# Kernel optimization log

Measured on AMD Instinct MI355X. Metric: run time of the kernel, lower is better.

## Reference

```python
import jax, jax.numpy as jnp
from jax import lax
import numpy as np

B, T, C, HID, H, W = 8, 24, 3, 32, 64, 64


def setup_inputs() -> dict:
    key = jax.random.key(0)
    ks = jax.random.split(key, 8)
    def n(k, shape, s=0.05):
        return jax.random.normal(k, shape, dtype=jnp.float32) * s
    return {
        "x": n(ks[0], (B, T, C, H, W), 1.0),
        # encoder layer 0: conv over concat(x, h) -> 4*HID gate channels
        "Wenc0": n(ks[1], (4 * HID, C + HID, 3, 3)),
        "benc0": jnp.zeros((4 * HID,), jnp.float32),
        # encoder layer 1: input is layer-0 hidden seq (HID channels)
        "Wenc1": n(ks[2], (4 * HID, HID + HID, 3, 3)),
        "benc1": jnp.zeros((4 * HID,), jnp.float32),
        # decoder (1 layer, input_dim channels in)
        "Wdec": n(ks[3], (4 * HID, C + HID, 3, 3)),
        "bdec": jnp.zeros((4 * HID,), jnp.float32),
        # MLP head: HID*H*W -> 256 -> 97
        "fc1_w": n(ks[4], (256, HID * H * W), 0.01),
        "fc1_b": jnp.zeros((256,), jnp.float32),
        "fc2_w": n(ks[5], (97, 256)),
        "fc2_b": jnp.zeros((97,), jnp.float32),
    }


def _cell_step(h, c, x_t, Wk, b):
    # ConvLSTM cell: conv(concat(x,h)) -> i,f,o,g gates
    z = lax.conv_general_dilated(
        jnp.concatenate([x_t, h], axis=1), Wk,
        window_strides=(1, 1), padding='SAME',
        dimension_numbers=('NCHW', 'OIHW', 'NCHW')) + b[None, :, None, None]
    i, f, o, g = jnp.split(z, 4, axis=1)
    c_new = jax.nn.sigmoid(f) * c + jax.nn.sigmoid(i) * jnp.tanh(g)
    h_new = jax.nn.sigmoid(o) * jnp.tanh(c_new)
    return h_new, c_new


def _run_layer(x_tb, Wk, b):
    # x_tb: [T, B, Cin, H, W]; zero-initialized state
    h0 = jnp.zeros((x_tb.shape[1], HID, H, W), x_tb.dtype)
    c0 = jnp.zeros_like(h0)
    def step(hc, xt):
        h, c = _cell_step(hc[0], hc[1], xt, Wk, b)
        return (h, c), h
    (hT, cT), hs = lax.scan(step, (h0, c0), x_tb)
    return hs, (hT, cT)


def reference(x, Wenc0, benc0, Wenc1, benc1, Wdec, bdec, fc1_w, fc1_b, fc2_w, fc2_b):
    x_tb = jnp.transpose(x, (1, 0, 2, 3, 4))          # [T,B,C,H,W]
    hs0, _ = _run_layer(x_tb, Wenc0, benc0)           # layer-0 hidden seq
    _, (hT, cT) = _run_layer(hs0, Wenc1, benc1)       # last-layer final state
    # decoder: one step on last input frame, seeded with encoder state
    h_dec, _ = _cell_step(hT, cT, x[:, -1], Wdec, bdec)  # [B,HID,H,W]
    feat = h_dec.reshape(h_dec.shape[0], -1)          # [B, HID*H*W]
    hdn = jax.nn.relu(feat @ fc1_w.T + fc1_b)
    return hdn @ fc2_w.T + fc2_b                      # [B, 97]
```

## Files before the change

### kernel.cpp

```cpp
#include <hip/hip_runtime.h>

typedef __attribute__((ext_vector_type(8))) short short8v;
typedef __attribute__((ext_vector_type(4))) float f32x4;
typedef __attribute__((ext_vector_type(4))) unsigned int uint4v;
typedef unsigned short u16;

__device__ __forceinline__ u16 f2bf(float f) {
  unsigned u = __float_as_uint(f);
  u += 0x7FFFu + ((u >> 16) & 1u);
  return (u16)(u >> 16);
}
__device__ __forceinline__ short8v ld8(const u16* p) {
  return *reinterpret_cast<const short8v*>(p);
}
__device__ __forceinline__ float frcp(float x) { return __builtin_amdgcn_rcpf(x); }

__device__ __forceinline__ void st_cg(u16* p, uint4v v) {
  asm volatile("global_store_dwordx4 %0, %1, off sc0 sc1" :: "v"(p), "v"(v) : "memory");
}
__device__ __forceinline__ void ld2_cg(const u16* a0, const u16* a1,
                                       uint4v& v0, uint4v& v1) {
  asm volatile(
      "global_load_dwordx4 %0, %2, off sc0 sc1\n\t"
      "global_load_dwordx4 %1, %3, off sc0 sc1\n\t"
      "s_waitcnt vmcnt(0)"
      : "=&v"(v0), "=&v"(v1) : "v"(a0), "v"(a1) : "memory");
}

__device__ __forceinline__ void poll_lane(const unsigned* a, unsigned tgt, bool active) {
  bool pending = active;
  while (__ballot(pending)) {
    if (pending &&
        __hip_atomic_load((unsigned*)a, __ATOMIC_RELAXED, __HIP_MEMORY_SCOPE_AGENT) >= tgt)
      pending = false;
    if (__ballot(pending)) __builtin_amdgcn_s_sleep(1);
  }
}
__device__ __forceinline__ void publish(unsigned* f, unsigned v) {
  __syncthreads();
  if (threadIdx.x == 0)
    __hip_atomic_store(f, v, __ATOMIC_RELAXED, __HIP_MEMORY_SCOPE_AGENT);
}

__global__ void k_pack(const float* __restrict__ We0, const float* __restrict__ We1,
                       const float* __restrict__ Wd,
                       u16* __restrict__ Wh0p, u16* __restrict__ Wx1p,
                       u16* __restrict__ Wh1p, u16* __restrict__ Whdp,
                       u16* __restrict__ Wx0p, u16* __restrict__ Wxdp,
                       unsigned* __restrict__ flags) {
  int i = blockIdx.x * 256 + threadIdx.x;
  if (i < 8192) flags[i] = 0u;
  if (i < 147456) {
    int tbl = i / 36864, j = i % 36864;
    int s = j >> 12, cg = (j >> 11) & 1, gate = (j >> 9) & 3,
        chl = (j >> 5) & 15, ci = j & 31;
    int co = gate * 32 + cg * 16 + chl;
    float v;
    if (tbl == 0)      v = We0[(co * 35 + 3 + ci) * 9 + s];
    else if (tbl == 1) v = We1[(co * 64 + ci) * 9 + s];
    else if (tbl == 2) v = We1[(co * 64 + 32 + ci) * 9 + s];
    else               v = Wd[(co * 35 + 3 + ci) * 9 + s];
    u16* dst = tbl == 0 ? Wh0p : tbl == 1 ? Wx1p : tbl == 2 ? Wh1p : Whdp;
    dst[j] = f2bf(v);
  } else {
    int j = i - 147456, tbl = j >> 12;
    j &= 4095;
    int cg = (j >> 11) & 1, gate = (j >> 9) & 3, chl = (j >> 5) & 15, k = j & 31;
    int co = gate * 32 + cg * 16 + chl;
    const float* src = tbl ? Wd : We0;
    u16 v = (k < 27) ? f2bf(src[(co * 35 + (k % 3)) * 9 + (k / 3)]) : (u16)0;
    (tbl ? Wxdp : Wx0p)[j] = v;
  }
}

__global__ void k_im2col(const float* __restrict__ x, u16* __restrict__ out) {
  int p = blockIdx.x * 256 + threadIdx.x;
  int t = p >> 15;
  int rem = p & 32767;
  int b = rem >> 12;
  int yy = (rem >> 6) & 63;
  int xx = rem & 63;
  __align__(16) u16 buf[32];
#pragma unroll
  for (int k = 27; k < 32; k++) buf[k] = 0;
  const float* xb = x + ((size_t)(b * 24 + t)) * 3 * 4096;
#pragma unroll
  for (int ky = 0; ky < 3; ky++) {
    int ys = yy + ky - 1;
    bool yok = (unsigned)ys < 64u;
#pragma unroll
    for (int kx = 0; kx < 3; kx++) {
      int xs = xx + kx - 1;
      bool ok = yok && ((unsigned)xs < 64u);
#pragma unroll
      for (int ci = 0; ci < 3; ci++) {
        float v = ok ? xb[(size_t)ci * 4096 + ys * 64 + xs] : 0.f;
        buf[(ky * 3 + kx) * 3 + ci] = f2bf(v);
      }
    }
  }
  uint4v* dst = (uint4v*)(out + (size_t)p * 32);
  const uint4v* s = (const uint4v*)buf;
  dst[0] = s[0]; dst[1] = s[1]; dst[2] = s[2]; dst[3] = s[3];
}

__global__ __launch_bounds__(512, 1) void k_persist(
    const u16* __restrict__ imc, u16* __restrict__ hs0G, u16* __restrict__ h1G,
    const u16* __restrict__ Wx0, const u16* __restrict__ Wh0,
    const float* __restrict__ be0,
    const u16* __restrict__ Wx1, const u16* __restrict__ Wh1,
    const float* __restrict__ be1,
    const u16* __restrict__ Wxd, const u16* __restrict__ Whd,
    const float* __restrict__ bd,
    float* __restrict__ hdec, unsigned* __restrict__ flag) {
  __shared__ __align__(16) u16 smH0[8448];
  __shared__ __align__(16) u16 smH1[8448];
  const int bid = blockIdx.x;
  const int b = bid & 7;
  const int yblk = bid >> 3;
  const int y0 = yblk << 1;
  const int fi = bid * 16;
  const int tid = threadIdx.x;
  const int w = tid >> 6, l = tid & 63, lr = l & 15, g = l >> 4;
  const bool isL1w = w >= 4;
  const int lw = w & 3, mh = lw >> 1, cg = lw & 1, y = y0 + mh;
  const int ch = cg * 16 + lr;

  if (tid < 64) {
    int q = tid & 31;
    int rgq = q >> 1, side = q & 1;
    u16* base = (tid < 32 ? smH0 : smH1) + ((size_t)(rgq * 66 + side * 65)) * 8;
    *(uint4v*)base = (uint4v)0u;
  }

  const float* bia = isL1w ? be1 : be0;
  const float bI = bia[ch], bF = bia[32 + ch], bO = bia[64 + ch], bG = bia[96 + ch];
  float cr[16];
#pragma unroll
  for (int i = 0; i < 16; i++) cr[i] = 0.f;

  const int sthr = tid & 255;
  const int sgrp = tid >> 8;
  const int pxs = sthr >> 2, gqs = sthr & 3;
  const size_t rbG = (size_t)b * 131072;
  const size_t poff = (size_t)pxs * 32 + gqs * 8;
  const int rup = (yblk == 0) ? y0 : y0 - 1;
  const int rdn = (yblk == 31) ? y0 + 1 : y0 + 2;
  u16* smS = sgrp ? smH1 : smH0;
  u16* dUp = smS + ((size_t)(gqs * 66 + pxs + 1)) * 8;
  u16* dDn = smS + ((size_t)((12 + gqs) * 66 + pxs + 1)) * 8;

  auto do_shifts = [&](const u16* sm, const u16* __restrict__ W, f32x4 (&acc)[4][4]) {
#pragma unroll
    for (int sft = 0; sft < 9; sft++) {
      const int ky = sft / 3, dx = sft % 3 - 1;
      const u16* wb = W + ((size_t)(sft * 2 + cg) * 64 + lr) * 32 + g * 8;
      short8v B0 = ld8(wb), B1 = ld8(wb + 512), B2 = ld8(wb + 1024), B3 = ld8(wb + 1536);
      const u16* abase = sm + ((size_t)(((mh + ky) * 4 + g) * 66 + lr + dx + 1)) * 8;
#pragma unroll
      for (int mt = 0; mt < 4; mt++) {
        short8v A = ld8(abase + mt * 128);
        acc[mt][0] = __builtin_amdgcn_mfma_f32_16x16x32_bf16(A, B0, acc[mt][0], 0, 0, 0);
        acc[mt][1] = __builtin_amdgcn_mfma_f32_16x16x32_bf16(A, B1, acc[mt][1], 0, 0, 0);
        acc[mt][2] = __builtin_amdgcn_mfma_f32_16x16x32_bf16(A, B2, acc[mt][2], 0, 0, 0);
        acc[mt][3] = __builtin_amdgcn_mfma_f32_16x16x32_bf16(A, B3, acc[mt][3], 0, 0, 0);
      }
    }
  };
  auto imcol = [&](const u16* xp, const u16* __restrict__ W, f32x4 (&acc)[4][4]) {
    const u16* ab = xp + rbG + (size_t)y * 2048 + g * 8;
    const u16* wb = W + ((size_t)(cg * 64 + lr)) * 32 + g * 8;
    short8v B0 = ld8(wb), B1 = ld8(wb + 512), B2 = ld8(wb + 1024), B3 = ld8(wb + 1536);
#pragma unroll
    for (int mt = 0; mt < 4; mt++) {
      short8v A = ld8(ab + (mt * 16 + lr) * 32);
      acc[mt][0] = __builtin_amdgcn_mfma_f32_16x16x32_bf16(A, B0, acc[mt][0], 0, 0, 0);
      acc[mt][1] = __builtin_amdgcn_mfma_f32_16x16x32_bf16(A, B1, acc[mt][1], 0, 0, 0);
      acc[mt][2] = __builtin_amdgcn_mfma_f32_16x16x32_bf16(A, B2, acc[mt][2], 0, 0, 0);
      acc[mt][3] = __builtin_amdgcn_mfma_f32_16x16x32_bf16(A, B3, acc[mt][3], 0, 0, 0);
    }
  };
  auto gates = [&](f32x4 (&acc)[4][4], u16* hbf) {
#pragma unroll
    for (int mt = 0; mt < 4; mt++) {
#pragma unroll
      for (int j = 0; j < 4; j++) {
        float zi = acc[mt][0][j] + bI, zf = acc[mt][1][j] + bF;
        float zo = acc[mt][2][j] + bO, zg = acc[mt][3][j] + bG;
        float ei = __expf(-zi), ef = __expf(-zf), eo = __expf(-zo);
        float eg = __expf(2.f * zg);
        float cn = frcp(1.f + ef) * cr[mt * 4 + j] +
                   (eg - 1.f) * frcp((1.f + ei) * (eg + 1.f));
        float ec = __expf(2.f * cn);
        cr[mt * 4 + j] = cn;
        hbf[mt * 4 + j] = f2bf((ec - 1.f) * frcp((1.f + eo) * (ec + 1.f)));
      }
    }
  };

  for (int s = 0; s <= 25; ++s) {
    if (s > 0 && tid < 64) {
      const unsigned* a = nullptr; bool act = false;
      if (l == 0 && yblk > 0)  { a = flag + fi - 128; act = true; }
      if (l == 1 && yblk < 31) { a = flag + fi + 128; act = true; }
      poll_lane(a, (unsigned)s, act);
    }
    __syncthreads();

    if (sgrp == 0 && s >= 1 && s <= 24) {
      const u16* src = hs0G + (size_t)((s - 1) & 1) * 1048576 + rbG;
      uint4v v0, v1;
      ld2_cg(src + (size_t)rup * 2048 + poff, src + (size_t)rdn * 2048 + poff, v0, v1);
      if (yblk == 0)  v0 = (uint4v)0u;
      if (yblk == 31) v1 = (uint4v)0u;
      *(uint4v*)dUp = v0; *(uint4v*)dDn = v1;
    }
    if (sgrp == 1 && s >= 2) {
      const u16* src = h1G + (size_t)(s & 1) * 1048576 + rbG;
      uint4v v0, v1;
      ld2_cg(src + (size_t)rup * 2048 + poff, src + (size_t)rdn * 2048 + poff, v0, v1);
      if (yblk == 0)  v0 = (uint4v)0u;
      if (yblk == 31) v1 = (uint4v)0u;
      *(uint4v*)dUp = v0; *(uint4v*)dDn = v1;
    }
    __syncthreads();

    if (s == 25) {
      if (isL1w) {
        f32x4 acc[4][4];
#pragma unroll
        for (int i = 0; i < 4; i++)
#pragma unroll
          for (int j = 0; j < 4; j++) acc[i][j] = (f32x4)0.f;
        imcol(imc + (size_t)23 * 1048576, Wxd, acc);
        do_shifts(smH1, Whd, acc);
        const float bId = bd[ch], bFd = bd[32 + ch], bOd = bd[64 + ch], bGd = bd[96 + ch];
#pragma unroll
        for (int mt = 0; mt < 4; mt++) {
#pragma unroll
          for (int j = 0; j < 4; j++) {
            int px = mt * 16 + g * 4 + j;
            float zi = acc[mt][0][j] + bId, zf = acc[mt][1][j] + bFd;
            float zo = acc[mt][2][j] + bOd, zg = acc[mt][3][j] + bGd;
            float ei = __expf(-zi), ef = __expf(-zf), eo = __expf(-zo);
            float eg = __expf(2.f * zg);
            float cn = frcp(1.f + ef) * cr[mt * 4 + j] +
                       (eg - 1.f) * frcp((1.f + ei) * (eg + 1.f));
            float ec = __expf(2.f * cn);
            float hn = (ec - 1.f) * frcp((1.f + eo) * (ec + 1.f));
            hdec[((size_t)(b * 32 + ch) * 64 + y) * 64 + px] = hn;
          }
        }
      }
      return;
    }

    const bool doL0 = !isL1w && s <= 23;
    const bool doL1 = isL1w && s >= 1 && s <= 24;
    u16 hbf[16];

    if (doL0) {
      f32x4 acc[4][4];
#pragma unroll
      for (int i = 0; i < 4; i++)
#pragma unroll
        for (int j = 0; j < 4; j++) acc[i][j] = (f32x4)0.f;
      imcol(imc + (size_t)s * 1048576, Wx0, acc);
      if (s >= 1) do_shifts(smH0, Wh0, acc);
      gates(acc, hbf);
    }
    if (doL1) {
      f32x4 acc[4][4];
#pragma unroll
      for (int i = 0; i < 4; i++)
#pragma unroll
        for (int j = 0; j < 4; j++) acc[i][j] = (f32x4)0.f;
      do_shifts(smH0, Wx1, acc);
      if (s >= 2) do_shifts(smH1, Wh1, acc);
      gates(acc, hbf);
    }
    __syncthreads();

    if (doL0 || doL1) {
      u16* smD = isL1w ? smH1 : smH0;
#pragma unroll
      for (int mt = 0; mt < 4; mt++)
#pragma unroll
        for (int j = 0; j < 4; j++) {
          int px = mt * 16 + g * 4 + j;
          smD[((size_t)((1 + mh) * 4 + (ch >> 3)) * 66 + px + 1) * 8 + (ch & 7)] =
              hbf[mt * 4 + j];
        }
    }
    __syncthreads();

    if (sgrp == 0 && s <= 23) {
      u16* d = hs0G + (size_t)(s & 1) * 1048576 + rbG;
      st_cg(d + (size_t)y0 * 2048 + poff,
            *(const uint4v*)(smH0 + ((size_t)(4 + gqs) * 66 + pxs + 1) * 8));
      st_cg(d + (size_t)(y0 + 1) * 2048 + poff,
            *(const uint4v*)(smH0 + ((size_t)(8 + gqs) * 66 + pxs + 1) * 8));
    }
    if (sgrp == 1 && s >= 1 && s <= 24) {
      u16* d = h1G + (size_t)((s - 1) & 1) * 1048576 + rbG;
      st_cg(d + (size_t)y0 * 2048 + poff,
            *(const uint4v*)(smH1 + ((size_t)(4 + gqs) * 66 + pxs + 1) * 8));
      st_cg(d + (size_t)(y0 + 1) * 2048 + poff,
            *(const uint4v*)(smH1 + ((size_t)(8 + gqs) * 66 + pxs + 1) * 8));
    }
    publish(flag + fi, (unsigned)(s + 1));
  }
}

__global__ __launch_bounds__(256) void k_fc1(const float* __restrict__ w,
                                             const float* __restrict__ feat,
                                             float* __restrict__ partial) {
  __shared__ float fsm[8][1024];
  const int ng = blockIdx.x, ks = blockIdx.y;
  const int tid = threadIdx.x;
  const float* fb = feat + (size_t)ks * 1024;
  for (int i = tid; i < 2048; i += 256) {
    int bb = i >> 8, kk = (i & 255) << 2;
    *(f32x4*)&fsm[bb][kk] = *(const f32x4*)(fb + (size_t)bb * 131072 + kk);
  }
  __syncthreads();
  const int wv = tid >> 6, lane = tid & 63;
  const int n0 = ng * 16 + wv * 4;
  const float* wr = w + (size_t)n0 * 131072 + (size_t)ks * 1024;
  float acc[4][8];
#pragma unroll
  for (int i = 0; i < 4; i++)
#pragma unroll
    for (int j = 0; j < 8; j++) acc[i][j] = 0.f;
#pragma unroll
  for (int it = 0; it < 4; it++) {
    int k = it * 256 + lane * 4;
    f32x4 w0 = *(const f32x4*)(wr + k);
    f32x4 w1 = *(const f32x4*)(wr + 131072 + k);
    f32x4 w2 = *(const f32x4*)(wr + 262144 + k);
    f32x4 w3 = *(const f32x4*)(wr + 393216 + k);
#pragma unroll
    for (int bb = 0; bb < 8; bb++) {
      f32x4 fv = *(const f32x4*)&fsm[bb][k];
      acc[0][bb] += w0[0] * fv[0] + w0[1] * fv[1] + w0[2] * fv[2] + w0[3] * fv[3];
      acc[1][bb] += w1[0] * fv[0] + w1[1] * fv[1] + w1[2] * fv[2] + w1[3] * fv[3];
      acc[2][bb] += w2[0] * fv[0] + w2[1] * fv[1] + w2[2] * fv[2] + w2[3] * fv[3];
      acc[3][bb] += w3[0] * fv[0] + w3[1] * fv[1] + w3[2] * fv[2] + w3[3] * fv[3];
    }
  }
#pragma unroll
  for (int nn = 0; nn < 4; nn++)
#pragma unroll
    for (int bb = 0; bb < 8; bb++) {
      float v = acc[nn][bb];
#pragma unroll
      for (int m = 32; m >= 1; m >>= 1) v += __shfl_xor(v, m, 64);
      if (lane == 0) partial[((size_t)ks * 8 + bb) * 256 + n0 + nn] = v;
    }
}

__global__ void k_fc1_fin(const float* __restrict__ partial,
                          const float* __restrict__ b1, float* __restrict__ hdn) {
  int i = blockIdx.x * 256 + threadIdx.x;
  if (i >= 2048) return;
  int b = i >> 8, n = i & 255;
  float v = b1[n];
  for (int ks = 0; ks < 128; ks++) v += partial[((size_t)ks * 8 + b) * 256 + n];
  hdn[i] = fmaxf(v, 0.f);
}

__global__ void k_fc2(const float* __restrict__ hdn, const float* __restrict__ w2,
                      const float* __restrict__ b2, float* __restrict__ out) {
  int i = blockIdx.x * 256 + threadIdx.x;
  if (i >= 776) return;
  int b = i / 97, m = i % 97;
  const float* h = hdn + b * 256;
  const float* wr = w2 + m * 256;
  float v = b2[m];
  for (int k = 0; k < 256; k++) v += h[k] * wr[k];
  out[i] = v;
}

extern "C" void kernel_launch(void* const* d_in, const int* in_sizes, int n_in,
                              void* d_out, int out_size, void* d_ws, size_t ws_size,
                              hipStream_t stream) {
  const float* x   = (const float*)d_in[0];
  const float* We0 = (const float*)d_in[1];
  const float* be0 = (const float*)d_in[2];
  const float* We1 = (const float*)d_in[3];
  const float* be1 = (const float*)d_in[4];
  const float* Wd  = (const float*)d_in[5];
  const float* bd  = (const float*)d_in[6];
  const float* f1w = (const float*)d_in[7];
  const float* f1b = (const float*)d_in[8];
  const float* f2w = (const float*)d_in[9];
  const float* f2b = (const float*)d_in[10];

  char* ws = (char*)d_ws;
  u16*      imc  = (u16*)(ws + 0);
  u16*      hs0G = (u16*)(ws + 50331648);
  u16*      h1G  = (u16*)(ws + 54525952);
  u16*      wp   = (u16*)(ws + 58720256);
  float*    hdec = (float*)(ws + 62914560);
  unsigned* flag = (unsigned*)(ws + 67108864);
  float*    part = (float*)(ws + 0);
  float*    hdn  = (float*)(ws + 1048576);
  u16 *Wh0p = wp, *Wx1p = wp + 36864, *Wh1p = wp + 73728, *Whdp = wp + 110592,
      *Wx0p = wp + 147456, *Wxdp = wp + 151552;

  k_pack<<<608, 256, 0, stream>>>(We0, We1, Wd, Wh0p, Wx1p, Wh1p, Whdp, Wx0p,
                                  Wxdp, flag);
  k_im2col<<<3072, 256, 0, stream>>>(x, imc);

  k_persist<<<256, 512, 0, stream>>>(imc, hs0G, h1G, Wx0p, Wh0p, be0,
                                     Wx1p, Wh1p, be1, Wxdp, Whdp, bd, hdec, flag);

  k_fc1<<<dim3(16, 128), 256, 0, stream>>>(f1w, hdec, part);
  k_fc1_fin<<<8, 256, 0, stream>>>(part, f1b, hdn);
  k_fc2<<<4, 256, 0, stream>>>(hdn, f2w, f2b, (float*)d_out);
}
```

Before: 335.6 us.

## Fuse im2col into persistent kernel with double-buffered LDS prefetch of next frame

Removes the separate im2col kernel and its 48MB bf16 intermediate buffer. Inside the persistent kernel, the 3x3x3 input patches for the next timestep are built from the fp32 input and written into a double-buffered LDS region, overlapping with the current step's work. This cuts a kernel launch and global memory traffic. In exchange it adds LDS usage and per-step gather work, including scattered global loads, inside the recurrent loop.

```diff
diff --git a/kernel.cpp b/kernel.cpp
--- a/kernel.cpp
+++ b/kernel.cpp
@@ -73,39 +73,8 @@
   }
 }
 
-__global__ void k_im2col(const float* __restrict__ x, u16* __restrict__ out) {
-  int p = blockIdx.x * 256 + threadIdx.x;
-  int t = p >> 15;
-  int rem = p & 32767;
-  int b = rem >> 12;
-  int yy = (rem >> 6) & 63;
-  int xx = rem & 63;
-  __align__(16) u16 buf[32];
-#pragma unroll
-  for (int k = 27; k < 32; k++) buf[k] = 0;
-  const float* xb = x + ((size_t)(b * 24 + t)) * 3 * 4096;
-#pragma unroll
-  for (int ky = 0; ky < 3; ky++) {
-    int ys = yy + ky - 1;
-    bool yok = (unsigned)ys < 64u;
-#pragma unroll
-    for (int kx = 0; kx < 3; kx++) {
-      int xs = xx + kx - 1;
-      bool ok = yok && ((unsigned)xs < 64u);
-#pragma unroll
-      for (int ci = 0; ci < 3; ci++) {
-        float v = ok ? xb[(size_t)ci * 4096 + ys * 64 + xs] : 0.f;
-        buf[(ky * 3 + kx) * 3 + ci] = f2bf(v);
-      }
-    }
-  }
-  uint4v* dst = (uint4v*)(out + (size_t)p * 32);
-  const uint4v* s = (const uint4v*)buf;
-  dst[0] = s[0]; dst[1] = s[1]; dst[2] = s[2]; dst[3] = s[3];
-}
-
 __global__ __launch_bounds__(512, 1) void k_persist(
-    const u16* __restrict__ imc, u16* __restrict__ hs0G, u16* __restrict__ h1G,
+    const float* __restrict__ xg, u16* __restrict__ hs0G, u16* __restrict__ h1G,
     const u16* __restrict__ Wx0, const u16* __restrict__ Wh0,
     const float* __restrict__ be0,
     const u16* __restrict__ Wx1, const u16* __restrict__ Wh1,
@@ -115,6 +84,7 @@
     float* __restrict__ hdec, unsigned* __restrict__ flag) {
   __shared__ __align__(16) u16 smH0[8448];
   __shared__ __align__(16) u16 smH1[8448];
+  __shared__ __align__(16) u16 smX[8448];
   const int bid = blockIdx.x;
   const int b = bid & 7;
   const int yblk = bid >> 3;
@@ -126,13 +96,6 @@
   const int lw = w & 3, mh = lw >> 1, cg = lw & 1, y = y0 + mh;
   const int ch = cg * 16 + lr;
 
-  if (tid < 64) {
-    int q = tid & 31;
-    int rgq = q >> 1, side = q & 1;
-    u16* base = (tid < 32 ? smH0 : smH1) + ((size_t)(rgq * 66 + side * 65)) * 8;
-    *(uint4v*)base = (uint4v)0u;
-  }
-
   const float* bia = isL1w ? be1 : be0;
   const float bI = bia[ch], bF = bia[32 + ch], bO = bia[64 + ch], bG = bia[96 + ch];
   float cr[16];
@@ -150,6 +113,27 @@
   u16* dUp = smS + ((size_t)(gqs * 66 + pxs + 1)) * 8;
   u16* dDn = smS + ((size_t)((12 + gqs) * 66 + pxs + 1)) * 8;
 
+  auto prefetch_x = [&](int t) {
+    const float* xb = xg + ((size_t)(b * 24 + t)) * 3 * 4096;
+    const int yr = y0 + sgrp;
+    __align__(16) u16 buf[8];
+#pragma unroll
+    for (int kk = 0; kk < 8; kk++) {
+      int k = gqs * 8 + kk;
+      float v = 0.f;
+      if (k < 27) {
+        int si = k / 3, ci = k - si * 3;
+        int ky = si / 3, kx = si - ky * 3;
+        int ys = yr + ky - 1, xs = pxs + kx - 1;
+        if ((unsigned)ys < 64u && (unsigned)xs < 64u)
+          v = xb[(size_t)ci * 4096 + ys * 64 + xs];
+      }
+      buf[kk] = f2bf(v);
+    }
+    *(uint4v*)(smX + ((size_t)(((t & 1) * 8 + sgrp * 4 + gqs) * 66 + pxs)) * 8) =
+        *(const uint4v*)buf;
+  };
+
   auto do_shifts = [&](const u16* sm, const u16* __restrict__ W, f32x4 (&acc)[4][4]) {
 #pragma unroll
     for (int sft = 0; sft < 9; sft++) {
@@ -167,13 +151,13 @@
       }
     }
   };
-  auto imcol = [&](const u16* xp, const u16* __restrict__ W, f32x4 (&acc)[4][4]) {
-    const u16* ab = xp + rbG + (size_t)y * 2048 + g * 8;
+  auto imcolX = [&](int par, const u16* __restrict__ W, f32x4 (&acc)[4][4]) {
+    const u16* ab = smX + ((size_t)((par * 8 + mh * 4 + g) * 66)) * 8;
     const u16* wb = W + ((size_t)(cg * 64 + lr)) * 32 + g * 8;
     short8v B0 = ld8(wb), B1 = ld8(wb + 512), B2 = ld8(wb + 1024), B3 = ld8(wb + 1536);
 #pragma unroll
     for (int mt = 0; mt < 4; mt++) {
-      short8v A = ld8(ab + (mt * 16 + lr) * 32);
+      short8v A = ld8(ab + ((size_t)(mt * 16 + lr)) * 8);
       acc[mt][0] = __builtin_amdgcn_mfma_f32_16x16x32_bf16(A, B0, acc[mt][0], 0, 0, 0);
       acc[mt][1] = __builtin_amdgcn_mfma_f32_16x16x32_bf16(A, B1, acc[mt][1], 0, 0, 0);
       acc[mt][2] = __builtin_amdgcn_mfma_f32_16x16x32_bf16(A, B2, acc[mt][2], 0, 0, 0);
@@ -198,6 +182,14 @@
     }
   };
 
+  if (tid < 64) {
+    int q = tid & 31;
+    int rgq = q >> 1, side = q & 1;
+    u16* base = (tid < 32 ? smH0 : smH1) + ((size_t)(rgq * 66 + side * 65)) * 8;
+    *(uint4v*)base = (uint4v)0u;
+  }
+  prefetch_x(0);
+
   for (int s = 0; s <= 25; ++s) {
     if (s > 0 && tid < 64) {
       const unsigned* a = nullptr; bool act = false;
@@ -223,6 +215,7 @@
       if (yblk == 31) v1 = (uint4v)0u;
       *(uint4v*)dUp = v0; *(uint4v*)dDn = v1;
     }
+    if (s <= 22) prefetch_x(s + 1);
     __syncthreads();
 
     if (s == 25) {
@@ -232,7 +225,7 @@
         for (int i = 0; i < 4; i++)
 #pragma unroll
           for (int j = 0; j < 4; j++) acc[i][j] = (f32x4)0.f;
-        imcol(imc + (size_t)23 * 1048576, Wxd, acc);
+        imcolX(1, Wxd, acc);
         do_shifts(smH1, Whd, acc);
         const float bId = bd[ch], bFd = bd[32 + ch], bOd = bd[64 + ch], bGd = bd[96 + ch];
 #pragma unroll
@@ -265,7 +258,7 @@
       for (int i = 0; i < 4; i++)
 #pragma unroll
         for (int j = 0; j < 4; j++) acc[i][j] = (f32x4)0.f;
-      imcol(imc + (size_t)s * 1048576, Wx0, acc);
+      imcolX(s & 1, Wx0, acc);
       if (s >= 1) do_shifts(smH0, Wh0, acc);
       gates(acc, hbf);
     }
@@ -397,7 +390,6 @@
   const float* f2b = (const float*)d_in[10];
 
   char* ws = (char*)d_ws;
-  u16*      imc  = (u16*)(ws + 0);
   u16*      hs0G = (u16*)(ws + 50331648);
   u16*      h1G  = (u16*)(ws + 54525952);
   u16*      wp   = (u16*)(ws + 58720256);
@@ -410,9 +402,8 @@
 
   k_pack<<<608, 256, 0, stream>>>(We0, We1, Wd, Wh0p, Wx1p, Wh1p, Whdp, Wx0p,
                                   Wxdp, flag);
-  k_im2col<<<3072, 256, 0, stream>>>(x, imc);
-
-  k_persist<<<256, 512, 0, stream>>>(imc, hs0G, h1G, Wx0p, Wh0p, be0,
+
+  k_persist<<<256, 512, 0, stream>>>(x, hs0G, h1G, Wx0p, Wh0p, be0,
                                      Wx1p, Wh1p, be1, Wxdp, Whdp, bd, hdec, flag);
 
   k_fc1<<<dim3(16, 128), 256, 0, stream>>>(f1w, hdec, part);
```

Result: slower. 373.2 us (+11.2%).
